# Kernel optimization log

Measured on AMD Instinct MI355X. Metric: run time of the kernel, lower is better.

Reference implementation:

```python
import jax, jax.numpy as jnp
import numpy as np

NUM_HEADS = 16
HEAD_SIZE = 64
MAX_POS = 2048  # config.max_position_embeddings


def setup_inputs() -> dict:
    key = jax.random.key(0)
    ks = jax.random.split(key, 8)
    B, Lq, Lk, D = 4, 1024, 2048, 1024
    s = 1.0 / np.sqrt(D)
    return {
        "hidden_states": jax.random.normal(ks[0], (B, Lk, D), jnp.float32),
        "query_hidden_states": jax.random.normal(ks[1], (B, Lq, D), jnp.float32),
        "attention_mask": jnp.zeros((B, 1, 1, Lk), jnp.float32),
        "Wq": jax.random.normal(ks[2], (D, D), jnp.float32) * s,
        "bq": jnp.zeros((D,), jnp.float32),
        "Wk": jax.random.normal(ks[3], (D, D), jnp.float32) * s,
        "bk": jnp.zeros((D,), jnp.float32),
        "Wv": jax.random.normal(ks[4], (D, D), jnp.float32) * s,
        "bv": jnp.zeros((D,), jnp.float32),
        "dist_emb": jax.random.normal(ks[5], (2 * MAX_POS - 1, HEAD_SIZE), jnp.float32) * 0.02,
    }


def _split_heads(x):
    # [B, L, H*Dh] -> [B, H, L, Dh]
    B, L, _ = x.shape
    return x.reshape(B, L, NUM_HEADS, HEAD_SIZE).transpose(0, 2, 1, 3)


def reference(hidden_states, query_hidden_states, attention_mask, Wq, bq, Wk, bk, Wv, bv, dist_emb):
    # Linear projections (torch Linear: x @ W.T + b)
    q = _split_heads(query_hidden_states @ Wq.T + bq)   # [B,H,Lq,Dh]
    k = _split_heads(hidden_states @ Wk.T + bk)          # [B,H,Lk,Dh]
    v = _split_heads(hidden_states @ Wv.T + bv)          # [B,H,Lk,Dh]

    scores = jnp.einsum('bhld,bhrd->bhlr', q, k)         # [B,H,Lq,Lk]

    # relative_key_query positional scores
    Lq, Lk = q.shape[2], k.shape[2]
    distance = jnp.arange(Lq)[:, None] - jnp.arange(Lk)[None, :]
    pe = dist_emb[distance + MAX_POS - 1]                # [Lq,Lk,Dh]
    scores = scores + jnp.einsum('bhld,lrd->bhlr', q, pe) + jnp.einsum('bhrd,lrd->bhlr', k, pe)

    scores = scores / np.sqrt(HEAD_SIZE) + attention_mask
    probs = jax.nn.softmax(scores, axis=-1)              # dropout p=0 (eval)
    ctx = jnp.einsum('bhlr,bhrd->bhld', probs, v)        # [B,H,Lq,Dh]
    B = ctx.shape[0]
    return ctx.transpose(0, 2, 1, 3).reshape(B, Lq, NUM_HEADS * HEAD_SIZE)
```

## Files before the change

### kernel.cpp

```cpp
#include <hip/hip_runtime.h>
#include <hip/hip_bf16.h>

#define B_   4
#define H_   16
#define LQ   1024
#define LK   2048
#define D_   1024
#define DH   64

typedef __attribute__((ext_vector_type(8))) short  short8;
typedef __attribute__((ext_vector_type(4))) float  float4_;
typedef __attribute__((ext_vector_type(4))) unsigned int uint4_;

static __device__ __forceinline__ float bf2f(unsigned short u) {
    unsigned int x = ((unsigned int)u) << 16;
    return __builtin_bit_cast(float, x);
}
static __device__ __forceinline__ unsigned short f2bf(float f) {
    unsigned int x = __builtin_bit_cast(unsigned int, f);
    unsigned int lsb = (x >> 16) & 1u;
    x += 0x7fffu + lsb;
    return (unsigned short)(x >> 16);
}
static __device__ __forceinline__ unsigned int pack2(float a, float b) {
    __hip_bfloat162 h = __float22bfloat162_rn(make_float2(a, b));
    unsigned int r;
    __builtin_memcpy(&r, &h, 4);
    return r;
}

#define MFMA(a, b, c) __builtin_amdgcn_mfma_f32_16x16x32_bf16((a), (b), (c), 0, 0, 0)

#define G2ROW(tl) ((tl) * 144 + ((tl) >> 2) * 8)

__global__ __launch_bounds__(256) void conv_kernel(
    const float* __restrict__ Wq, const float* __restrict__ Wk,
    const float* __restrict__ Wv, const float* __restrict__ Eg,
    unsigned short* __restrict__ cWq, unsigned short* __restrict__ cWk,
    unsigned short* __restrict__ cWv, unsigned short* __restrict__ cEb)
{
    int bid = blockIdx.x;
    const float* src; unsigned short* dst; int nch;
    if (bid < 512)       { src = Wq; dst = cWq;              nch = 131072; }
    else if (bid < 1024) { src = Wk; dst = cWk; bid -= 512;  nch = 131072; }
    else if (bid < 1536) { src = Wv; dst = cWv; bid -= 1024; nch = 131072; }
    else                 { src = Eg; dst = cEb; bid -= 1536; nch = 32760;  }
    int ch = bid * 256 + threadIdx.x;
    if (ch >= nch) return;
    const float* s = src + (size_t)ch * 8;
    float4_ v0 = *(const float4_*)s, v1 = *(const float4_*)(s + 4);
    uint4_ o;
    o[0] = pack2(v0[0], v0[1]); o[1] = pack2(v0[2], v0[3]);
    o[2] = pack2(v1[0], v1[1]); o[3] = pack2(v1[2], v1[3]);
    *(uint4_*)(dst + (size_t)ch * 8) = o;
}

__global__ __launch_bounds__(256) void proj_kernel(
    const float* __restrict__ Xq, const float* __restrict__ Xk,
    const unsigned short* __restrict__ Wq, const float* __restrict__ bq,
    const unsigned short* __restrict__ Wk, const float* __restrict__ bk,
    const unsigned short* __restrict__ Wv, const float* __restrict__ bv,
    unsigned short* __restrict__ Qh, unsigned short* __restrict__ Kh,
    unsigned short* __restrict__ VT)
{
    __shared__ short smem[17408];
    short* As = smem;
    short* Bs = smem + 5120;
    short* Cs = smem;

    int bid = blockIdx.x;
    int which, tm, tn;
    const float *X, *bias; const unsigned short* W;
    if (bid < 256)      { which = 0; int t = bid;       tm = t >> 3; tn = t & 7; X = Xq; W = Wq; bias = bq; }
    else if (bid < 768) { which = 1; int t = bid - 256; tm = t >> 3; tn = t & 7; X = Xk; W = Wk; bias = bk; }
    else                { which = 2; int t = bid - 768; tm = t >> 3; tn = t & 7; X = Xk; W = Wv; bias = bv; }

    int tid  = threadIdx.x;
    int wave = tid >> 6, lane = tid & 63;
    int wr = (wave >> 1) * 64, wc = (wave & 1) * 64;
    int m0 = tm * 128, n0 = tn * 128;

    float4_ acc[4][4];
    for (int a = 0; a < 4; ++a) for (int c = 0; c < 4; ++c) acc[a][c] = (float4_)0.0f;

    int srow = tid >> 2, skp = (tid & 3) * 8;
    const float*          Ag = X + (size_t)(m0 + srow) * D_ + skp;
    const unsigned short* Bg = W + (size_t)(n0 + srow) * D_ + skp;
    int lrow = lane & 15, lk8 = (lane >> 4) * 8;

    float4_ pa0[2], pa1[2]; uint4_ pb[2];
    auto load_kt = [&](int kt) {
        int k0 = kt * 32;
        #pragma unroll
        for (int i = 0; i < 2; ++i) {
            const float* pa = Ag + (size_t)i * 64 * D_ + k0;
            pa0[i] = *(const float4_*)(pa);
            pa1[i] = *(const float4_*)(pa + 4);
            pb[i]  = *(const uint4_*)(Bg + (size_t)i * 64 * D_ + k0);
        }
    };
    load_kt(0);

    for (int kt = 0; kt < 32; ++kt) {
        __syncthreads();
        #pragma unroll
        for (int i = 0; i < 2; ++i) {
            int row = srow + i * 64;
            uint4_ va;
            va[0] = pack2(pa0[i][0], pa0[i][1]); va[1] = pack2(pa0[i][2], pa0[i][3]);
            va[2] = pack2(pa1[i][0], pa1[i][1]); va[3] = pack2(pa1[i][2], pa1[i][3]);
            *(uint4_*)(&As[row * 40 + skp]) = va;
            *(uint4_*)(&Bs[row * 40 + skp]) = pb[i];
        }
        __syncthreads();
        if (kt < 31) load_kt(kt + 1);
        short8 af[4], bfr[4];
        for (int rt = 0; rt < 4; ++rt) af[rt]  = *(const short8*)(&As[(wr + rt * 16 + lrow) * 40 + lk8]);
        for (int ct = 0; ct < 4; ++ct) bfr[ct] = *(const short8*)(&Bs[(wc + ct * 16 + lrow) * 40 + lk8]);
        for (int rt = 0; rt < 4; ++rt)
            for (int ct = 0; ct < 4; ++ct)
                acc[rt][ct] = MFMA(af[rt], bfr[ct], acc[rt][ct]);
    }
    __syncthreads();

    int lrow4 = (lane >> 4) * 4, lcol = lane & 15;
    if (which < 2) {
        int lsh = (which == 0) ? 10 : 11;
        int Lm1 = (1 << lsh) - 1;
        unsigned short* dst = (which == 0) ? Qh : Kh;
        for (int rt = 0; rt < 4; ++rt)
            for (int ct = 0; ct < 4; ++ct)
                for (int i = 0; i < 4; ++i) {
                    int m = m0 + wr + rt * 16 + lrow4 + i;
                    int n = n0 + wc + ct * 16 + lcol;
                    float v = acc[rt][ct][i] + bias[n];
                    int b = m >> lsh, s = m & Lm1;
                    int h = n >> 6, d = n & 63;
                    dst[((size_t)((b * H_ + h) << lsh) + (size_t)s) * DH + d] = f2bf(v);
                }
    } else {
        for (int rt = 0; rt < 4; ++rt)
            for (int ct = 0; ct < 4; ++ct)
                for (int i = 0; i < 4; ++i) {
                    int rl = wr + rt * 16 + lrow4 + i;
                    int cl = wc + ct * 16 + lcol;
                    float v = acc[rt][ct][i] + bias[n0 + cl];
                    Cs[cl * 136 + rl] = (short)f2bf(v);
                }
        __syncthreads();
        int b = m0 >> 11, r0 = m0 & 2047;
        int c = tid >> 1, half = tid & 1;
        int n = n0 + c, h = n >> 6, d = n & 63;
        unsigned short* dstp = VT + ((size_t)(b * H_ + h) * DH + d) * LK + r0 + half * 64;
        for (int j = 0; j < 8; ++j) {
            uint4_ v = *(const uint4_*)(&Cs[c * 136 + half * 64 + j * 8]);
            *(uint4_*)(dstp + j * 8) = v;
        }
    }
}

__global__ __launch_bounds__(256, 2) void attn_kernel(
    const unsigned short* __restrict__ Qh, const unsigned short* __restrict__ Kh,
    const unsigned short* __restrict__ VT, const unsigned short* __restrict__ Eb,
    const float* __restrict__ mask, float* __restrict__ out)
{
    __shared__ short smem[27776];
    short* Qs  = smem;
    short* Ks  = smem;
    short* VTs = smem + 4608;
    short* Es  = smem + 9216;
    short* G2  = smem + 18432;
    short* Ps  = G2;

    int bid = blockIdx.x;
    int l0 = (bid & 15) * 64;
    int bh = bid >> 4;
    int b  = bh >> 4, h = bh & 15;
    int tid = threadIdx.x, wave = tid >> 6, lane = tid & 63;
    int lr = lane & 15, lk8 = (lane >> 4) * 8, lr4 = (lane >> 4) * 4;

    for (int i = 0; i < 2; ++i) {
        int idx = tid + 256 * i, row = idx >> 3, g = (idx & 7) * 8;
        *(uint4_*)(&Qs[row * 72 + g]) =
            *(const uint4_*)(Qh + ((size_t)(bh * LQ + l0 + row)) * DH + g);
    }
    __syncthreads();
    short8 aq0 = *(const short8*)(&Qs[(wave * 16 + lr) * 72 + lk8]);
    short8 aq1 = *(const short8*)(&Qs[(wave * 16 + lr) * 72 + 32 + lk8]);

    float m_i[4], l_i[4];
    float4_ Oacc[4];
    for (int i = 0; i < 4; ++i) { m_i[i] = -1e30f; l_i[i] = 0.f; Oacc[i] = (float4_)0.f; }

    const unsigned short* Kbase = Kh + (size_t)bh * LK * DH;
    const unsigned short* Vbase = VT + (size_t)bh * DH * LK;

    int srow = tid >> 3;
    int sg   = (tid & 7) * 8;

    uint4_ kr0, kr1, vr0, vr1, er0, er1, er2, er3;
    auto load_tiles = [&](int it2) {
        int r0_ = it2 * 64, jb_ = l0 - r0_ + 1984;
        kr0 = *(const uint4_*)(Kbase + (size_t)(r0_ + srow) * DH + sg);
        kr1 = *(const uint4_*)(Kbase + (size_t)(r0_ + srow + 32) * DH + sg);
        vr0 = *(const uint4_*)(Vbase + (size_t)srow * LK + r0_ + sg);
        vr1 = *(const uint4_*)(Vbase + (size_t)(srow + 32) * LK + r0_ + sg);
        er0 = *(const uint4_*)(Eb + (size_t)(jb_ + srow) * DH + sg);
        er1 = *(const uint4_*)(Eb + (size_t)(jb_ + srow + 32) * DH + sg);
    };
    load_tiles(0);
    {
        int jb0 = l0 + 1984;
        er2 = *(const uint4_*)(Eb + (size_t)(jb0 + srow + 64) * DH + sg);
        er3 = *(const uint4_*)(Eb + (size_t)(jb0 + srow + 96) * DH + sg);
    }

    for (int it = 0; it < 32; ++it) {
        int r0 = it * 64;
        int ph = (l0 + 1984 - r0) & 127;

        __syncthreads();
        *(uint4_*)(&Ks[srow * 72 + sg])         = kr0;
        *(uint4_*)(&Ks[(srow + 32) * 72 + sg])  = kr1;
        *(uint4_*)(&VTs[srow * 72 + sg])        = vr0;
        *(uint4_*)(&VTs[(srow + 32) * 72 + sg]) = vr1;
        *(uint4_*)(&Es[((ph + srow) & 127) * 72 + sg])      = er0;
        *(uint4_*)(&Es[((ph + srow + 32) & 127) * 72 + sg]) = er1;
        if (it == 0) {
            *(uint4_*)(&Es[((ph + srow + 64) & 127) * 72 + sg]) = er2;
            *(uint4_*)(&Es[((ph + srow + 96) & 127) * 72 + sg]) = er3;
        }
        __syncthreads();
        if (it < 31) load_tiles(it + 1);

        short8 ak0, ak1;
        float4_ Sacc[4];
        #pragma unroll
        for (int c = 0; c < 4; ++c) {
            short8 b0 = *(const short8*)(&Ks[(c * 16 + lr) * 72 + lk8]);
            short8 b1 = *(const short8*)(&Ks[(c * 16 + lr) * 72 + 32 + lk8]);
            float4_ s = (float4_)0.f;
            s = MFMA(aq0, b0, s);
            s = MFMA(aq1, b1, s);
            Sacc[c] = s;
            if (c == 0 || c == wave) { ak0 = b0; ak1 = b1; }
        }

        #pragma unroll
        for (int t = 0; t < 8; ++t) {
            int dq = t - wave;
            int dk = t - 3 + wave;
            bool needq = (unsigned)dq < 5u;
            bool needk = (unsigned)dk < 5u;
            if (!(needq || needk)) continue;
            int es = ((ph + t * 16 + lr) & 127) * 72;
            short8 e0 = *(const short8*)(&Es[es + lk8]);
            short8 e1 = *(const short8*)(&Es[es + 32 + lk8]);
            int u = t * 16 + lr;
            if (needq) {
                float4_ g = (float4_)0.f;
                g = MFMA(aq0, e0, g); g = MFMA(aq1, e1, g);
                unsigned int p0 = pack2(g[0], g[1]), p1 = pack2(g[2], g[3]);
                #pragma unroll
                for (int i = 0; i < 4; ++i) {
                    int row = wave * 16 + lr4 + i;
                    unsigned int w32 = (i >> 1) ? p1 : p0;
                    unsigned short vq = (unsigned short)((i & 1) ? (w32 >> 16) : (w32 & 0xffff));
                    int tr = row - u + 63;
                    if ((unsigned)tr < 64u)
                        G2[G2ROW(row) + ((tr & 15) << 3) + ((tr >> 4) << 1)] = (short)vq;
                }
            }
            if (needk) {
                float4_ gg = (float4_)0.f;
                gg = MFMA(ak0, e0, gg); gg = MFMA(ak1, e1, gg);
                unsigned int q0 = pack2(gg[0], gg[1]), q1 = pack2(gg[2], gg[3]);
                #pragma unroll
                for (int i = 0; i < 4; ++i) {
                    int row = wave * 16 + lr4 + i;
                    unsigned int w32 = (i >> 1) ? q1 : q0;
                    unsigned short vk = (unsigned short)((i & 1) ? (w32 >> 16) : (w32 & 0xffff));
                    int tl = u + row - 63;
                    if ((unsigned)tl < 64u)
                        G2[G2ROW(tl) + ((row & 15) << 3) + ((row >> 4) << 1) + 1] = (short)vk;
                }
            }
        }
        __syncthreads();

        float mk[4];
        for (int c = 0; c < 4; ++c) mk[c] = mask[b * LK + r0 + c * 16 + lr];
        for (int i = 0; i < 4; ++i) {
            int tl = wave * 16 + lr4 + i;
            short8 gv = *(const short8*)(&G2[G2ROW(tl) + (lr << 3)]);
            float scv[4], mx = -1e30f;
            for (int c = 0; c < 4; ++c) {
                float sq = bf2f((unsigned short)gv[2 * c]);
                float sk = bf2f((unsigned short)gv[2 * c + 1]);
                float sc = (Sacc[c][i] + sq + sk) * 0.125f + mk[c];
                scv[c] = sc;
                mx = fmaxf(mx, sc);
            }
            for (int off = 1; off < 16; off <<= 1) mx = fmaxf(mx, __shfl_xor(mx, off, 64));
            float mnew = fmaxf(m_i[i], mx);
            float alpha = __expf(m_i[i] - mnew);
            m_i[i] = mnew;
            float e0 = __expf(scv[0] - mnew), e1 = __expf(scv[1] - mnew);
            float e2 = __expf(scv[2] - mnew), e3 = __expf(scv[3] - mnew);
            unsigned int p01 = pack2(e0, e1), p23 = pack2(e2, e3);
            float rs = bf2f((unsigned short)(p01 & 0xffff)) + bf2f((unsigned short)(p01 >> 16))
                     + bf2f((unsigned short)(p23 & 0xffff)) + bf2f((unsigned short)(p23 >> 16));
            for (int off = 1; off < 16; off <<= 1) rs += __shfl_xor(rs, off, 64);
            l_i[i] = l_i[i] * alpha + rs;
            for (int nt = 0; nt < 4; ++nt) Oacc[nt][i] *= alpha;
            Ps[G2ROW(tl) +  0 + lr] = (short)(unsigned short)(p01 & 0xffff);
            Ps[G2ROW(tl) + 16 + lr] = (short)(unsigned short)(p01 >> 16);
            Ps[G2ROW(tl) + 32 + lr] = (short)(unsigned short)(p23 & 0xffff);
            Ps[G2ROW(tl) + 48 + lr] = (short)(unsigned short)(p23 >> 16);
        }
        short8 ap0 = *(const short8*)(&Ps[G2ROW(wave * 16 + lr) + lk8]);
        short8 ap1 = *(const short8*)(&Ps[G2ROW(wave * 16 + lr) + 32 + lk8]);
        for (int nt = 0; nt < 4; ++nt) {
            short8 v0 = *(const short8*)(&VTs[(nt * 16 + lr) * 72 + lk8]);
            short8 v1 = *(const short8*)(&VTs[(nt * 16 + lr) * 72 + 32 + lk8]);
            Oacc[nt] = MFMA(ap0, v0, Oacc[nt]);
            Oacc[nt] = MFMA(ap1, v1, Oacc[nt]);
        }
    }

    for (int nt = 0; nt < 4; ++nt)
        for (int i = 0; i < 4; ++i) {
            int row = l0 + wave * 16 + lr4 + i;
            int col = h * 64 + nt * 16 + lr;
            out[(size_t)(b * LQ + row) * D_ + col] = Oacc[nt][i] / l_i[i];
        }
}

extern "C" void kernel_launch(void* const* d_in, const int* in_sizes, int n_in,
                              void* d_out, int out_size, void* d_ws, size_t ws_size,
                              hipStream_t stream) {
    (void)in_sizes; (void)n_in; (void)out_size; (void)ws_size;
    const float* Xk   = (const float*)d_in[0];
    const float* Xq   = (const float*)d_in[1];
    const float* mask = (const float*)d_in[2];
    const float* Wq   = (const float*)d_in[3];
    const float* bq   = (const float*)d_in[4];
    const float* Wk   = (const float*)d_in[5];
    const float* bk   = (const float*)d_in[6];
    const float* Wv   = (const float*)d_in[7];
    const float* bv   = (const float*)d_in[8];
    const float* Eg   = (const float*)d_in[9];

    unsigned short* Qh  = (unsigned short*)d_ws;
    unsigned short* Kh  = Qh  + (size_t)4194304;
    unsigned short* VT  = Kh  + (size_t)8388608;
    unsigned short* cWq = VT  + (size_t)8388608;
    unsigned short* cWk = cWq + (size_t)1048576;
    unsigned short* cWv = cWk + (size_t)1048576;
    unsigned short* cEb = cWv + (size_t)1048576;
    float* o = (float*)d_out;

    conv_kernel<<<1664, 256, 0, stream>>>(Wq, Wk, Wv, Eg, cWq, cWk, cWv, cEb);
    proj_kernel<<<1280, 256, 0, stream>>>(Xq, Xk, cWq, bq, cWk, bk, cWv, bv, Qh, Kh, VT);
    attn_kernel<<<1024, 256, 0, stream>>>(Qh, Kh, VT, cEb, mask, o);
}
```

Baseline: 487.3 us.

## Shrink attention LDS footprint to fit three workgroups per CU

Replaces the swizzled G2 positional-score buffer with a padded row-stride-65 packed q/k layout, and moves the probability tile into the now-unused half of the ring-buffered embedding region. This trims shared memory so launch bounds can request three workgroups per CU instead of two, aiming to hide latency through higher occupancy. The risk is register pressure from the tighter launch bound, possible spills, bank conflicts from the new 4-byte-strided reads, and correctness dependence on that Es region being dead when P is written.

```diff
diff --git a/kernel.cpp b/kernel.cpp
--- a/kernel.cpp
+++ b/kernel.cpp
@@ -30,8 +30,6 @@
 }
 
 #define MFMA(a, b, c) __builtin_amdgcn_mfma_f32_16x16x32_bf16((a), (b), (c), 0, 0, 0)
-
-#define G2ROW(tl) ((tl) * 144 + ((tl) >> 2) * 8)
 
 __global__ __launch_bounds__(256) void conv_kernel(
     const float* __restrict__ Wq, const float* __restrict__ Wk,
@@ -159,18 +157,19 @@
     }
 }
 
-__global__ __launch_bounds__(256, 2) void attn_kernel(
+__global__ __launch_bounds__(256, 3) void attn_kernel(
     const unsigned short* __restrict__ Qh, const unsigned short* __restrict__ Kh,
     const unsigned short* __restrict__ VT, const unsigned short* __restrict__ Eb,
     const float* __restrict__ mask, float* __restrict__ out)
 {
-    __shared__ short smem[27776];
+    __shared__ short smem[26752];
     short* Qs  = smem;
     short* Ks  = smem;
     short* VTs = smem + 4608;
     short* Es  = smem + 9216;
-    short* G2  = smem + 18432;
-    short* Ps  = G2;
+    unsigned int* Gqk = (unsigned int*)(smem + 18432);
+    short* Gs  = smem + 18432;
+    short* Ps  = Es;
 
     int bid = blockIdx.x;
     int l0 = (bid & 15) * 64;
@@ -266,9 +265,9 @@
                     int row = wave * 16 + lr4 + i;
                     unsigned int w32 = (i >> 1) ? p1 : p0;
                     unsigned short vq = (unsigned short)((i & 1) ? (w32 >> 16) : (w32 & 0xffff));
-                    int tr = row - u + 63;
-                    if ((unsigned)tr < 64u)
-                        G2[G2ROW(row) + ((tr & 15) << 3) + ((tr >> 4) << 1)] = (short)vq;
+                    int j = row - u + 63;
+                    if ((unsigned)j < 64u)
+                        Gs[(row * 65 + j) * 2] = (short)vq;
                 }
             }
             if (needk) {
@@ -277,12 +276,12 @@
                 unsigned int q0 = pack2(gg[0], gg[1]), q1 = pack2(gg[2], gg[3]);
                 #pragma unroll
                 for (int i = 0; i < 4; ++i) {
-                    int row = wave * 16 + lr4 + i;
+                    int jk = wave * 16 + lr4 + i;
                     unsigned int w32 = (i >> 1) ? q1 : q0;
                     unsigned short vk = (unsigned short)((i & 1) ? (w32 >> 16) : (w32 & 0xffff));
-                    int tl = u + row - 63;
+                    int tl = u + jk - 63;
                     if ((unsigned)tl < 64u)
-                        G2[G2ROW(tl) + ((row & 15) << 3) + ((row >> 4) << 1) + 1] = (short)vk;
+                        Gs[(tl * 65 + jk) * 2 + 1] = (short)vk;
                 }
             }
         }
@@ -292,11 +291,14 @@
         for (int c = 0; c < 4; ++c) mk[c] = mask[b * LK + r0 + c * 16 + lr];
         for (int i = 0; i < 4; ++i) {
             int tl = wave * 16 + lr4 + i;
-            short8 gv = *(const short8*)(&G2[G2ROW(tl) + (lr << 3)]);
+            const unsigned int* gr = Gqk + tl * 65 + lr;
+            unsigned int gva[4];
+            gva[0] = gr[0]; gva[1] = gr[16]; gva[2] = gr[32]; gva[3] = gr[48];
             float scv[4], mx = -1e30f;
+            #pragma unroll
             for (int c = 0; c < 4; ++c) {
-                float sq = bf2f((unsigned short)gv[2 * c]);
-                float sk = bf2f((unsigned short)gv[2 * c + 1]);
+                float sq = bf2f((unsigned short)(gva[c] & 0xffff));
+                float sk = bf2f((unsigned short)(gva[c] >> 16));
                 float sc = (Sacc[c][i] + sq + sk) * 0.125f + mk[c];
                 scv[c] = sc;
                 mx = fmaxf(mx, sc);
@@ -313,13 +315,15 @@
             for (int off = 1; off < 16; off <<= 1) rs += __shfl_xor(rs, off, 64);
             l_i[i] = l_i[i] * alpha + rs;
             for (int nt = 0; nt < 4; ++nt) Oacc[nt][i] *= alpha;
-            Ps[G2ROW(tl) +  0 + lr] = (short)(unsigned short)(p01 & 0xffff);
-            Ps[G2ROW(tl) + 16 + lr] = (short)(unsigned short)(p01 >> 16);
-            Ps[G2ROW(tl) + 32 + lr] = (short)(unsigned short)(p23 & 0xffff);
-            Ps[G2ROW(tl) + 48 + lr] = (short)(unsigned short)(p23 >> 16);
-        }
-        short8 ap0 = *(const short8*)(&Ps[G2ROW(wave * 16 + lr) + lk8]);
-        short8 ap1 = *(const short8*)(&Ps[G2ROW(wave * 16 + lr) + 32 + lk8]);
+            int pr = ((ph + 64 + tl) & 127) * 72;
+            Ps[pr +  0 + lr] = (short)(unsigned short)(p01 & 0xffff);
+            Ps[pr + 16 + lr] = (short)(unsigned short)(p01 >> 16);
+            Ps[pr + 32 + lr] = (short)(unsigned short)(p23 & 0xffff);
+            Ps[pr + 48 + lr] = (short)(unsigned short)(p23 >> 16);
+        }
+        int par = ((ph + 64 + wave * 16 + lr) & 127) * 72;
+        short8 ap0 = *(const short8*)(&Ps[par + lk8]);
+        short8 ap1 = *(const short8*)(&Ps[par + 32 + lk8]);
         for (int nt = 0; nt < 4; ++nt) {
             short8 v0 = *(const short8*)(&VTs[(nt * 16 + lr) * 72 + lk8]);
             short8 v1 = *(const short8*)(&VTs[(nt * 16 + lr) * 72 + 32 + lk8]);
```

After: 715.2 us. 1.47x slower.
